# Kernel optimization log

Measured on AMD Instinct MI355X. Metric: run time of the kernel, lower is better.

## Reference

```python
import jax, jax.numpy as jnp
import numpy as np
import math

D_MODEL = 1024
N_HEADS = 16
HEAD_DIM = D_MODEL // N_HEADS
BAND_RADIUS = 2
BAND_VAL = 0.1


def setup_inputs() -> dict:
    key = jax.random.key(0)
    ks = jax.random.split(key, 12)
    B, S = 4, 2048
    scale = 1.0 / math.sqrt(D_MODEL)
    inp = {
        "x": jax.random.normal(ks[0], (B, S, D_MODEL), dtype=jnp.float32),
        "ocr_context": jax.random.normal(ks[1], (B, S, D_MODEL), dtype=jnp.float32),
        "Wq": jax.random.normal(ks[2], (D_MODEL, D_MODEL), dtype=jnp.float32) * scale,
        "bq": jnp.zeros((D_MODEL,), dtype=jnp.float32),
        "Wk": jax.random.normal(ks[3], (D_MODEL, D_MODEL), dtype=jnp.float32) * scale,
        "bk": jnp.zeros((D_MODEL,), dtype=jnp.float32),
        "Wv": jax.random.normal(ks[4], (D_MODEL, D_MODEL), dtype=jnp.float32) * scale,
        "bv": jnp.zeros((D_MODEL,), dtype=jnp.float32),
        "Wo": jax.random.normal(ks[5], (D_MODEL, D_MODEL), dtype=jnp.float32) * scale,
        "bo": jnp.zeros((D_MODEL,), dtype=jnp.float32),
        "ocr_bias": jax.random.normal(ks[6], (D_MODEL,), dtype=jnp.float32),
    }
    return inp


def _band_mask(S, dtype):
    # additive mask: 0.1 inside |i-j| <= 2, else 0 (matches _create_ocr_pattern_mask)
    i = jnp.arange(S)
    band = (jnp.abs(i[:, None] - i[None, :]) <= BAND_RADIUS).astype(dtype) * BAND_VAL
    return band[None, None, :, :]  # [1,1,S,S], broadcasts over batch & heads


def reference(x, ocr_context, Wq, bq, Wk, bk, Wv, bv, Wo, bo, ocr_bias):
    B, S, _ = x.shape
    # torch Linear: x @ W.T + b
    q = x @ Wq.T + bq + ocr_bias  # ocr bias added to q before head split
    k = x @ Wk.T + bk
    v = x @ Wv.T + bv
    q = q.reshape(B, S, N_HEADS, HEAD_DIM).transpose(0, 2, 1, 3)  # [B,H,S,d]
    k = k.reshape(B, S, N_HEADS, HEAD_DIM).transpose(0, 2, 1, 3)
    v = v.reshape(B, S, N_HEADS, HEAD_DIM).transpose(0, 2, 1, 3)
    scores = jnp.einsum("bhsd,bhtd->bhst", q, k) / math.sqrt(HEAD_DIM)
    scores = scores + _band_mask(S, scores.dtype)  # ocr_context only supplies shape
    attn = jax.nn.softmax(scores, axis=-1)
    out = jnp.einsum("bhst,bhtd->bhsd", attn, v)
    out = out.transpose(0, 2, 1, 3).reshape(B, S, D_MODEL)
    return out @ Wo.T + bo
```

## Files before the change

kernel.cpp:

```cpp
#include <hip/hip_runtime.h>
#include <hip/hip_bf16.h>
#include <stdint.h>

typedef __attribute__((ext_vector_type(8))) short bf16x8;
typedef __attribute__((ext_vector_type(4))) float f32x4;
typedef __attribute__((ext_vector_type(16))) float f32x16;
typedef __attribute__((ext_vector_type(4))) unsigned u32x4;

#define L2E 1.4426950408889634f

static __device__ __forceinline__ unsigned short f2bf(float f) {
    __hip_bfloat16 h = __float2bfloat16(f);
    return __builtin_bit_cast(unsigned short, h);
}

static __device__ __forceinline__ void gl2lds16(const void* g, void* l) {
    __builtin_amdgcn_global_load_lds(
        (const __attribute__((address_space(1))) void*)g,
        (__attribute__((address_space(3))) void*)l,
        16, 0, 0);
}

__global__ void cast_kernel(const float* __restrict__ src,
                            unsigned short* __restrict__ dst, int n4) {
    int i = blockIdx.x * blockDim.x + threadIdx.x;
    int stride = gridDim.x * blockDim.x;
    for (; i < n4; i += stride) {
        float4 v = ((const float4*)src)[i];
        ushort4 o;
        o.x = f2bf(v.x); o.y = f2bf(v.y); o.z = f2bf(v.z); o.w = f2bf(v.w);
        ((ushort4*)dst)[i] = o;
    }
}

__global__ void cast4_kernel(const float* __restrict__ s0, const float* __restrict__ s1,
                             const float* __restrict__ s2, const float* __restrict__ s3,
                             unsigned short* __restrict__ d0, unsigned short* __restrict__ d1,
                             unsigned short* __restrict__ d2, unsigned short* __restrict__ d3) {
    const int m = blockIdx.y;
    const float* src = m == 0 ? s0 : m == 1 ? s1 : m == 2 ? s2 : s3;
    unsigned short* dst = m == 0 ? d0 : m == 1 ? d1 : m == 2 ? d2 : d3;
    int i = blockIdx.x * blockDim.x + threadIdx.x;
    for (; i < 262144; i += 256 * 256) {
        float4 v = ((const float4*)src)[i];
        ushort4 o;
        o.x = f2bf(v.x); o.y = f2bf(v.y); o.z = f2bf(v.z); o.w = f2bf(v.w);
        ((ushort4*)dst)[i] = o;
    }
}

__global__ __launch_bounds__(256) void qkv_gemm(
    const unsigned short* __restrict__ A,
    const unsigned short* __restrict__ Wq,
    const unsigned short* __restrict__ Wk,
    const unsigned short* __restrict__ Wv,
    const float* __restrict__ bq,
    const float* __restrict__ bk,
    const float* __restrict__ bv,
    const float* __restrict__ ocr,
    float qscale,
    unsigned short* __restrict__ Qo,
    unsigned short* __restrict__ Ko,
    unsigned short* __restrict__ VTo)
{
    constexpr int K = 1024;
    __shared__ unsigned short As[128][64];
    __shared__ unsigned short Bs[128][64];

    const int tid  = threadIdx.x;
    const int wave = tid >> 6, lane = tid & 63;
    const int li = lane & 15, lg = lane >> 4;

    const int lin = blockIdx.y * 24 + blockIdx.x;
    const int n2  = (lin & 7) * 192 + (lin >> 3);
    const int mb = n2 / 24, nbb = n2 - mb * 24;
    const int proj = nbb >> 3;
    const int m0 = mb * 128, n0 = (nbb & 7) * 128;

    const unsigned short* W = proj == 0 ? Wq : proj == 1 ? Wk : Wv;
    const float* bias = proj == 0 ? bq : proj == 1 ? bk : bv;

    const int wm = (wave >> 1) * 64, wn = (wave & 1) * 64;
    const int srow = wave * 8 + (lane >> 3);
    const int scol = (lane & 7) * 8;

    f32x4 acc[4][4] = {};

    for (int k0 = 0; k0 < K; k0 += 64) {
#pragma unroll
        for (int rnd = 0; rnd < 4; ++rnd)
            gl2lds16(A + (size_t)(m0 + rnd * 32 + srow) * K + k0 + scol,
                     &As[rnd * 32 + wave * 8][0]);
#pragma unroll
        for (int rnd = 0; rnd < 4; ++rnd)
            gl2lds16(W + (size_t)(n0 + rnd * 32 + srow) * K + k0 + scol,
                     &Bs[rnd * 32 + wave * 8][0]);
        __syncthreads();
#pragma unroll
        for (int kk = 0; kk < 64; kk += 32) {
            bf16x8 af[4], bfr[4];
#pragma unroll
            for (int m = 0; m < 4; ++m)
                af[m] = *(const bf16x8*)&As[wm + m * 16 + li][kk + lg * 8];
#pragma unroll
            for (int n = 0; n < 4; ++n)
                bfr[n] = *(const bf16x8*)&Bs[wn + n * 16 + li][kk + lg * 8];
#pragma unroll
            for (int m = 0; m < 4; ++m)
#pragma unroll
                for (int n = 0; n < 4; ++n)
                    acc[m][n] = __builtin_amdgcn_mfma_f32_16x16x32_bf16(
                        af[m], bfr[n], acc[m][n], 0, 0, 0);
        }
        __syncthreads();
    }

    const float scale = proj == 0 ? qscale : 1.f;
#pragma unroll
    for (int n = 0; n < 4; ++n) {
        const int col = n0 + wn + n * 16 + li;
        float bb = bias[col];
        if (proj == 0) bb += ocr[col];
#pragma unroll
        for (int m = 0; m < 4; ++m) {
            if (proj == 2) {
                const int row0 = m0 + wm + m * 16 + lg * 4;
                size_t addr = ((size_t)(((row0 >> 11) << 4) + (col >> 6)) * 64 + (col & 63)) * 2048
                              + (row0 & 2047);
                ushort4 o;
                o.x = f2bf(acc[m][n][0] + bb);
                o.y = f2bf(acc[m][n][1] + bb);
                o.z = f2bf(acc[m][n][2] + bb);
                o.w = f2bf(acc[m][n][3] + bb);
                *(ushort4*)&VTo[addr] = o;
            } else {
                unsigned short* dst = proj == 0 ? Qo : Ko;
#pragma unroll
                for (int r = 0; r < 4; ++r) {
                    const int row = m0 + wm + m * 16 + lg * 4 + r;
                    dst[(size_t)row * 1024 + col] = f2bf((acc[m][n][r] + bb) * scale);
                }
            }
        }
    }
}

__global__ __launch_bounds__(256) void out_gemm(
    const unsigned short* __restrict__ A,
    const unsigned short* __restrict__ W,
    const float* __restrict__ bias,
    float* __restrict__ of)
{
    constexpr int K = 1024;
    __shared__ unsigned short As[128][64];
    __shared__ unsigned short Bs[128][64];

    const int tid  = threadIdx.x;
    const int wave = tid >> 6, lane = tid & 63;
    const int li = lane & 15, lg = lane >> 4;
    const int lin = blockIdx.y * 8 + blockIdx.x;
    const int n2  = (lin & 7) * 64 + (lin >> 3);
    const int m0 = (n2 >> 3) * 128, n0 = (n2 & 7) * 128;
    const int wm = (wave >> 1) * 64, wn = (wave & 1) * 64;

    const int srow = wave * 8 + (lane >> 3);
    const int scol = (lane & 7) * 8;

    f32x4 acc[4][4] = {};

    for (int k0 = 0; k0 < K; k0 += 64) {
#pragma unroll
        for (int rnd = 0; rnd < 4; ++rnd)
            gl2lds16(A + (size_t)(m0 + rnd * 32 + srow) * K + k0 + scol,
                     &As[rnd * 32 + wave * 8][0]);
#pragma unroll
        for (int rnd = 0; rnd < 4; ++rnd)
            gl2lds16(W + (size_t)(n0 + rnd * 32 + srow) * K + k0 + scol,
                     &Bs[rnd * 32 + wave * 8][0]);
        __syncthreads();
#pragma unroll
        for (int kk = 0; kk < 64; kk += 32) {
            bf16x8 af[4], bfr[4];
#pragma unroll
            for (int m = 0; m < 4; ++m)
                af[m] = *(const bf16x8*)&As[wm + m * 16 + li][kk + lg * 8];
#pragma unroll
            for (int n = 0; n < 4; ++n)
                bfr[n] = *(const bf16x8*)&Bs[wn + n * 16 + li][kk + lg * 8];
#pragma unroll
            for (int m = 0; m < 4; ++m)
#pragma unroll
                for (int n = 0; n < 4; ++n)
                    acc[m][n] = __builtin_amdgcn_mfma_f32_16x16x32_bf16(
                        af[m], bfr[n], acc[m][n], 0, 0, 0);
        }
        __syncthreads();
    }

#pragma unroll
    for (int n = 0; n < 4; ++n) {
        const int col = n0 + wn + n * 16 + li;
        const float bb = bias[col];
#pragma unroll
        for (int m = 0; m < 4; ++m)
#pragma unroll
            for (int r = 0; r < 4; ++r) {
                const int row = m0 + wm + m * 16 + lg * 4 + r;
                of[(size_t)row * 1024 + col] = acc[m][n][r] + bb;
            }
    }
}

__global__ __launch_bounds__(256, 2) void attn_kernel(
    const unsigned short* __restrict__ Q,
    const unsigned short* __restrict__ Km,
    const unsigned short* __restrict__ VT,
    unsigned short* __restrict__ AO)
{
    __shared__ unsigned short Ks[2][4096];
    __shared__ unsigned short Vs[2][4096];

    const int tid  = threadIdx.x;
    const int w = tid >> 6, lane = tid & 63;
    const int li5 = lane & 31, l5 = lane >> 5, li7 = li5 & 7;

    const int p  = blockIdx.y * 8 + blockIdx.x;
    const int q_ = (p & 7) * 64 + (p >> 3);
    const int bx = q_ & 7, bh = q_ >> 3;
    const int b = bh >> 4, h = bh & 15;
    const int qb = bx * 256 + w * 64;

    const int srow = w * 16 + (lane >> 3);
    const int swz  = ((lane & 7) ^ (lane >> 3)) * 8;

    const unsigned short* Kg0 = Km + (size_t)(b * 2048 + srow) * 1024 + h * 64 + swz;
    const unsigned short* Vg0 = VT + ((size_t)bh * 64 + srow) * 2048 + swz;

    bf16x8 qf[2][4];
#pragma unroll
    for (int s = 0; s < 2; ++s)
#pragma unroll
        for (int f = 0; f < 4; ++f)
            qf[s][f] = *(const bf16x8*)&Q[(size_t)(b * 2048 + qb + s * 32 + li5) * 1024
                                          + h * 64 + f * 16 + l5 * 8];

    f32x16 acc[2][2] = {};
    float ls00 = 0.f, ls01 = 0.f, ls10 = 0.f, ls11 = 0.f;

#pragma unroll
    for (int it = 0; it < 2; ++it) {
        gl2lds16(Kg0 + (size_t)(it * 8) * 1024, &Ks[0][(w * 2 + it) * 512]);
        gl2lds16(Vg0 + (size_t)(it * 8) * 2048, &Vs[0][(w * 2 + it) * 512]);
    }
    __syncthreads();

    for (int t = 0; t < 32; ++t) {
        const int buf = t & 1;
        const int j0 = t * 64;
        if (t < 31) {
            const int j1 = j0 + 64;
#pragma unroll
            for (int it = 0; it < 2; ++it) {
                gl2lds16(Kg0 + (size_t)(j1 + it * 8) * 1024, &Ks[buf ^ 1][(w * 2 + it) * 512]);
                gl2lds16(Vg0 + (size_t)(it * 8) * 2048 + j1, &Vs[buf ^ 1][(w * 2 + it) * 512]);
            }
        }

        bf16x8 kf[2][4];
#pragma unroll
        for (int jf = 0; jf < 2; ++jf)
#pragma unroll
            for (int f = 0; f < 4; ++f)
                kf[jf][f] = *(const bf16x8*)&Ks[buf][(jf * 32 + li5) * 64
                                                     + ((f * 2 + l5) ^ li7) * 8];

        unsigned pw[2][2][8];
#pragma unroll
        for (int s = 0; s < 2; ++s) {
            f32x16 st[2];
            __builtin_amdgcn_s_setprio(1);
#pragma unroll
            for (int jf = 0; jf < 2; ++jf) {
                f32x16 z = {};
#pragma unroll
                for (int f = 0; f < 4; ++f)
                    z = __builtin_amdgcn_mfma_f32_32x32x16_bf16(kf[jf][f], qf[s][f], z, 0, 0, 0);
                st[jf] = z;
            }
            __builtin_amdgcn_s_setprio(0);

            const int qbs = qb + s * 32;
            if (j0 >= qbs - 65 && j0 <= qbs + 33) {
#pragma unroll
                for (int jf = 0; jf < 2; ++jf)
#pragma unroll
                    for (int r = 0; r < 16; ++r) {
                        int j = j0 + jf * 32 + (r & 3) + 8 * (r >> 2) + 4 * l5;
                        int dq = (qbs + li5) - j;
                        if ((unsigned)(dq + 2) <= 4u) st[jf][r] += 0.1f * L2E;
                    }
            }

#pragma unroll
            for (int jf = 0; jf < 2; ++jf)
#pragma unroll
                for (int m = 0; m < 8; ++m) {
                    float p0 = __builtin_amdgcn_exp2f(st[jf][2 * m]);
                    float p1 = __builtin_amdgcn_exp2f(st[jf][2 * m + 1]);
                    float pp = p0 + p1;
                    if (s == 0) { if (m & 1) ls01 += pp; else ls00 += pp; }
                    else        { if (m & 1) ls11 += pp; else ls10 += pp; }
                    asm("v_cvt_pk_bf16_f32 %0, %1, %2"
                        : "=v"(pw[s][jf][m]) : "v"(p0), "v"(p1));
                }

#pragma unroll
            for (int jf = 0; jf < 2; ++jf)
#pragma unroll
                for (int m2 = 0; m2 < 2; ++m2)
#pragma unroll
                    for (int m0_ = 0; m0_ < 2; ++m0_) {
                        unsigned a0 = pw[s][jf][m2 * 4 + m0_];
                        unsigned b0 = pw[s][jf][m2 * 4 + m0_ + 2];
                        asm volatile("v_permlane32_swap_b32 %0, %1"
                                     : "+v"(a0), "+v"(b0));
                        pw[s][jf][m2 * 4 + m0_]     = a0;
                        pw[s][jf][m2 * 4 + m0_ + 2] = b0;
                    }
        }

        __builtin_amdgcn_s_setprio(1);
#pragma unroll
        for (int db = 0; db < 2; ++db)
#pragma unroll
            for (int tt = 0; tt < 4; ++tt) {
                bf16x8 vf = *(const bf16x8*)&Vs[buf][(db * 32 + li5) * 64
                                                     + ((tt * 2 + l5) ^ li7) * 8];
                const int jf = tt >> 1, m2 = tt & 1;
#pragma unroll
                for (int s = 0; s < 2; ++s) {
                    u32x4 tw = {pw[s][jf][m2 * 4 + 0], pw[s][jf][m2 * 4 + 1],
                                pw[s][jf][m2 * 4 + 2], pw[s][jf][m2 * 4 + 3]};
                    acc[s][db] = __builtin_amdgcn_mfma_f32_32x32x16_bf16(
                        vf, __builtin_bit_cast(bf16x8, tw), acc[s][db], 0, 0, 0);
                }
            }
        __builtin_amdgcn_s_setprio(0);
        __syncthreads();
    }

#pragma unroll
    for (int s = 0; s < 2; ++s) {
        float lr = s == 0 ? (ls00 + ls01) : (ls10 + ls11);
        float l2 = lr + __shfl_xor(lr, 32);
        const float inv = 1.f / l2;
        const int qrow = qb + s * 32 + li5;
#pragma unroll
        for (int db = 0; db < 2; ++db)
#pragma unroll
            for (int g = 0; g < 4; ++g) {
                ushort4 o;
                o.x = f2bf(acc[s][db][g * 4 + 0] * inv);
                o.y = f2bf(acc[s][db][g * 4 + 1] * inv);
                o.z = f2bf(acc[s][db][g * 4 + 2] * inv);
                o.w = f2bf(acc[s][db][g * 4 + 3] * inv);
                *(ushort4*)&AO[(size_t)(b * 2048 + qrow) * 1024 + h * 64
                               + db * 32 + g * 8 + l5 * 4] = o;
            }
    }
}

extern "C" void kernel_launch(void* const* d_in, const int* in_sizes, int n_in,
                              void* d_out, int out_size, void* d_ws, size_t ws_size,
                              hipStream_t stream) {
    const float* x   = (const float*)d_in[0];
    const float* Wq  = (const float*)d_in[2];
    const float* bq  = (const float*)d_in[3];
    const float* Wk  = (const float*)d_in[4];
    const float* bk  = (const float*)d_in[5];
    const float* Wv  = (const float*)d_in[6];
    const float* bv  = (const float*)d_in[7];
    const float* Wo  = (const float*)d_in[8];
    const float* bo  = (const float*)d_in[9];
    const float* ocr = (const float*)d_in[10];
    float* out = (float*)d_out;

    char* ws = (char*)d_ws;
    const size_t MB = 1024 * 1024;
    unsigned short* xb  = (unsigned short*)(ws);
    unsigned short* Wqb = (unsigned short*)(ws + 16 * MB);
    unsigned short* Wkb = (unsigned short*)(ws + 18 * MB);
    unsigned short* Wvb = (unsigned short*)(ws + 20 * MB);
    unsigned short* Wob = (unsigned short*)(ws + 22 * MB);
    unsigned short* Qb  = (unsigned short*)(ws + 24 * MB);
    unsigned short* Kb  = (unsigned short*)(ws + 40 * MB);
    unsigned short* VTb = (unsigned short*)(ws + 56 * MB);
    unsigned short* AO  = xb;

    cast_kernel<<<2048, 256, 0, stream>>>(x, xb, 8388608 / 4);
    cast4_kernel<<<dim3(256, 4), 256, 0, stream>>>(Wq, Wk, Wv, Wo,
                                                   Wqb, Wkb, Wvb, Wob);

    const float QSC = 0.125f * L2E;
    qkv_gemm<<<dim3(24, 64), 256, 0, stream>>>(xb, Wqb, Wkb, Wvb,
                                               bq, bk, bv, ocr, QSC,
                                               Qb, Kb, VTb);

    attn_kernel<<<dim3(8, 64), 256, 0, stream>>>(Qb, Kb, VTb, AO);

    out_gemm<<<dim3(8, 64), 256, 0, stream>>>(AO, Wob, bo, out);
}
```

Before: 193.3 us.

## Software-pipeline attention PV across iterations and stage V-transpose stores through LDS

The attention loop is unrolled by four with compile-time buffer indices. The P·V MFMA for tile t-1 now runs during iteration t, using a 4-deep V buffer and double-buffered P registers, so the softmax exp work can overlap the previous tile's matrix ops. Separately, the QKV GEMM epilogue for V writes the transposed tile into swizzled LDS first and then emits coalesced 16-byte stores, replacing the scattered 8-byte transposed global writes. The trade-off is more registers and LDS in the attention kernel, which may reduce occupancy, plus an extra barrier in the GEMM epilogue.

Result: slower. 555.5 us (+187.4%).

```diff
diff --git a/kernel.cpp b/kernel.cpp
--- a/kernel.cpp
+++ b/kernel.cpp
@@ -1,6 +1,7 @@
 #include <hip/hip_runtime.h>
 #include <hip/hip_bf16.h>
 #include <stdint.h>
+#include <type_traits>
 
 typedef __attribute__((ext_vector_type(8))) short bf16x8;
 typedef __attribute__((ext_vector_type(4))) float f32x4;
@@ -64,8 +65,9 @@
     unsigned short* __restrict__ VTo)
 {
     constexpr int K = 1024;
-    __shared__ unsigned short As[128][64];
-    __shared__ unsigned short Bs[128][64];
+    __shared__ __align__(16) unsigned short SMEM[16384];
+    unsigned short (*As)[64] = (unsigned short(*)[64])SMEM;
+    unsigned short (*Bs)[64] = (unsigned short(*)[64])(SMEM + 8192);
 
     const int tid  = threadIdx.x;
     const int wave = tid >> 6, lane = tid & 63;
@@ -115,32 +117,54 @@
         __syncthreads();
     }
 
-    const float scale = proj == 0 ? qscale : 1.f;
-#pragma unroll
-    for (int n = 0; n < 4; ++n) {
-        const int col = n0 + wn + n * 16 + li;
-        float bb = bias[col];
-        if (proj == 0) bb += ocr[col];
-#pragma unroll
-        for (int m = 0; m < 4; ++m) {
-            if (proj == 2) {
-                const int row0 = m0 + wm + m * 16 + lg * 4;
-                size_t addr = ((size_t)(((row0 >> 11) << 4) + (col >> 6)) * 64 + (col & 63)) * 2048
-                              + (row0 & 2047);
+    if (proj == 2) {
+#pragma unroll
+        for (int n = 0; n < 4; ++n) {
+            const int dl = wn + n * 16 + li;
+            const float bb = bias[n0 + dl];
+#pragma unroll
+            for (int m = 0; m < 4; ++m) {
+                const int sl = wm + m * 16 + lg * 4;
+                const int unit = (sl >> 2) ^ (dl & 7);
                 ushort4 o;
                 o.x = f2bf(acc[m][n][0] + bb);
                 o.y = f2bf(acc[m][n][1] + bb);
                 o.z = f2bf(acc[m][n][2] + bb);
                 o.w = f2bf(acc[m][n][3] + bb);
-                *(ushort4*)&VTo[addr] = o;
-            } else {
-                unsigned short* dst = proj == 0 ? Qo : Ko;
+                *(ushort4*)&SMEM[dl * 128 + unit * 4] = o;
+            }
+        }
+        __syncthreads();
+        const int s2 = (lane & 15) * 8;
+        const int u0b = s2 >> 2;
+#pragma unroll
+        for (int k = 0; k < 8; ++k) {
+            const int dl = wave * 32 + k * 4 + (lane >> 4);
+            const int u0 = u0b ^ (dl & 7);
+            const int u1 = (u0b + 1) ^ (dl & 7);
+            uint2 lo = *(uint2*)&SMEM[dl * 128 + u0 * 4];
+            uint2 hi = *(uint2*)&SMEM[dl * 128 + u1 * 4];
+            const int col = n0 + dl;
+            const int bh2 = ((m0 >> 11) << 4) + (col >> 6);
+            uint4 o4;
+            o4.x = lo.x; o4.y = lo.y; o4.z = hi.x; o4.w = hi.y;
+            *(uint4*)&VTo[((size_t)bh2 * 64 + (col & 63)) * 2048 + (m0 & 2047) + s2] = o4;
+        }
+    } else {
+        const float scale = proj == 0 ? qscale : 1.f;
+        unsigned short* dst = proj == 0 ? Qo : Ko;
+#pragma unroll
+        for (int n = 0; n < 4; ++n) {
+            const int col = n0 + wn + n * 16 + li;
+            float bb = bias[col];
+            if (proj == 0) bb += ocr[col];
+#pragma unroll
+            for (int m = 0; m < 4; ++m)
 #pragma unroll
                 for (int r = 0; r < 4; ++r) {
                     const int row = m0 + wm + m * 16 + lg * 4 + r;
                     dst[(size_t)row * 1024 + col] = f2bf((acc[m][n][r] + bb) * scale);
                 }
-            }
         }
     }
 }
@@ -218,7 +242,7 @@
     unsigned short* __restrict__ AO)
 {
     __shared__ unsigned short Ks[2][4096];
-    __shared__ unsigned short Vs[2][4096];
+    __shared__ unsigned short Vs[4][4096];
 
     const int tid  = threadIdx.x;
     const int w = tid >> 6, lane = tid & 63;
@@ -246,6 +270,7 @@
 
     f32x16 acc[2][2] = {};
     float ls00 = 0.f, ls01 = 0.f, ls10 = 0.f, ls11 = 0.f;
+    unsigned pw[2][2][2][8];
 
 #pragma unroll
     for (int it = 0; it < 2; ++it) {
@@ -254,15 +279,17 @@
     }
     __syncthreads();
 
-    for (int t = 0; t < 32; ++t) {
-        const int buf = t & 1;
-        const int j0 = t * 64;
-        if (t < 31) {
+    auto iter = [&](auto Uc, int t_) {
+        constexpr int U = decltype(Uc)::value;
+        const int j0 = t_ * 64;
+        if (t_ < 31) {
             const int j1 = j0 + 64;
 #pragma unroll
             for (int it = 0; it < 2; ++it) {
-                gl2lds16(Kg0 + (size_t)(j1 + it * 8) * 1024, &Ks[buf ^ 1][(w * 2 + it) * 512]);
-                gl2lds16(Vg0 + (size_t)(it * 8) * 2048 + j1, &Vs[buf ^ 1][(w * 2 + it) * 512]);
+                gl2lds16(Kg0 + (size_t)(j1 + it * 8) * 1024,
+                         &Ks[(U + 1) & 1][(w * 2 + it) * 512]);
+                gl2lds16(Vg0 + (size_t)(it * 8) * 2048 + j1,
+                         &Vs[(U + 1) & 3][(w * 2 + it) * 512]);
             }
         }
 
@@ -271,10 +298,9 @@
         for (int jf = 0; jf < 2; ++jf)
 #pragma unroll
             for (int f = 0; f < 4; ++f)
-                kf[jf][f] = *(const bf16x8*)&Ks[buf][(jf * 32 + li5) * 64
-                                                     + ((f * 2 + l5) ^ li7) * 8];
-
-        unsigned pw[2][2][8];
+                kf[jf][f] = *(const bf16x8*)&Ks[U & 1][(jf * 32 + li5) * 64
+                                                       + ((f * 2 + l5) ^ li7) * 8];
+
 #pragma unroll
         for (int s = 0; s < 2; ++s) {
             f32x16 st[2];
@@ -311,7 +337,7 @@
                     if (s == 0) { if (m & 1) ls01 += pp; else ls00 += pp; }
                     else        { if (m & 1) ls11 += pp; else ls10 += pp; }
                     asm("v_cvt_pk_bf16_f32 %0, %1, %2"
-                        : "=v"(pw[s][jf][m]) : "v"(p0), "v"(p1));
+                        : "=v"(pw[U & 1][s][jf][m]) : "v"(p0), "v"(p1));
                 }
 
 #pragma unroll
@@ -320,34 +346,69 @@
                 for (int m2 = 0; m2 < 2; ++m2)
 #pragma unroll
                     for (int m0_ = 0; m0_ < 2; ++m0_) {
-                        unsigned a0 = pw[s][jf][m2 * 4 + m0_];
-                        unsigned b0 = pw[s][jf][m2 * 4 + m0_ + 2];
+                        unsigned a0 = pw[U & 1][s][jf][m2 * 4 + m0_];
+                        unsigned b0 = pw[U & 1][s][jf][m2 * 4 + m0_ + 2];
                         asm volatile("v_permlane32_swap_b32 %0, %1"
                                      : "+v"(a0), "+v"(b0));
-                        pw[s][jf][m2 * 4 + m0_]     = a0;
-                        pw[s][jf][m2 * 4 + m0_ + 2] = b0;
+                        pw[U & 1][s][jf][m2 * 4 + m0_]     = a0;
+                        pw[U & 1][s][jf][m2 * 4 + m0_ + 2] = b0;
                     }
         }
 
-        __builtin_amdgcn_s_setprio(1);
-#pragma unroll
-        for (int db = 0; db < 2; ++db)
-#pragma unroll
-            for (int tt = 0; tt < 4; ++tt) {
-                bf16x8 vf = *(const bf16x8*)&Vs[buf][(db * 32 + li5) * 64
-                                                     + ((tt * 2 + l5) ^ li7) * 8];
-                const int jf = tt >> 1, m2 = tt & 1;
-#pragma unroll
-                for (int s = 0; s < 2; ++s) {
-                    u32x4 tw = {pw[s][jf][m2 * 4 + 0], pw[s][jf][m2 * 4 + 1],
-                                pw[s][jf][m2 * 4 + 2], pw[s][jf][m2 * 4 + 3]};
-                    acc[s][db] = __builtin_amdgcn_mfma_f32_32x32x16_bf16(
-                        vf, __builtin_bit_cast(bf16x8, tw), acc[s][db], 0, 0, 0);
+        if (t_ > 0) {
+            __builtin_amdgcn_s_setprio(1);
+#pragma unroll
+            for (int db = 0; db < 2; ++db)
+#pragma unroll
+                for (int tt = 0; tt < 4; ++tt) {
+                    bf16x8 vf = *(const bf16x8*)&Vs[(U + 3) & 3][(db * 32 + li5) * 64
+                                                                 + ((tt * 2 + l5) ^ li7) * 8];
+                    const int jf = tt >> 1, m2 = tt & 1;
+#pragma unroll
+                    for (int s = 0; s < 2; ++s) {
+                        u32x4 tw;
+                        tw.x = pw[(U + 1) & 1][s][jf][m2 * 4 + 0];
+                        tw.y = pw[(U + 1) & 1][s][jf][m2 * 4 + 1];
+                        tw.z = pw[(U + 1) & 1][s][jf][m2 * 4 + 2];
+                        tw.w = pw[(U + 1) & 1][s][jf][m2 * 4 + 3];
+                        acc[s][db] = __builtin_amdgcn_mfma_f32_32x32x16_bf16(
+                            vf, __builtin_bit_cast(bf16x8, tw), acc[s][db], 0, 0, 0);
+                    }
                 }
-            }
-        __builtin_amdgcn_s_setprio(0);
-        __syncthreads();
-    }
+            __builtin_amdgcn_s_setprio(0);
+        }
+        __syncthreads();
+    };
+
+#pragma unroll 1
+    for (int i = 0; i < 8; ++i) {
+        const int t4 = i * 4;
+        iter(std::integral_constant<int, 0>{}, t4 + 0);
+        iter(std::integral_constant<int, 1>{}, t4 + 1);
+        iter(std::integral_constant<int, 2>{}, t4 + 2);
+        iter(std::integral_constant<int, 3>{}, t4 + 3);
+    }
+
+    __builtin_amdgcn_s_setprio(1);
+#pragma unroll
+    for (int db = 0; db < 2; ++db)
+#pragma unroll
+        for (int tt = 0; tt < 4; ++tt) {
+            bf16x8 vf = *(const bf16x8*)&Vs[3][(db * 32 + li5) * 64
+                                             + ((tt * 2 + l5) ^ li7) * 8];
+            const int jf = tt >> 1, m2 = tt & 1;
+#pragma unroll
+            for (int s = 0; s < 2; ++s) {
+                u32x4 tw;
+                tw.x = pw[1][s][jf][m2 * 4 + 0];
+                tw.y = pw[1][s][jf][m2 * 4 + 1];
+                tw.z = pw[1][s][jf][m2 * 4 + 2];
+                tw.w = pw[1][s][jf][m2 * 4 + 3];
+                acc[s][db] = __builtin_amdgcn_mfma_f32_32x32x16_bf16(
+                    vf, __builtin_bit_cast(bf16x8, tw), acc[s][db], 0, 0, 0);
+            }
+        }
+    __builtin_amdgcn_s_setprio(0);
 
 #pragma unroll
     for (int s = 0; s < 2; ++s) {
```
